# Performance work log

Measured on AMD Instinct MI355X. Metric: run time of the kernel, lower is better.

Reference implementation:

```python
import jax, jax.numpy as jnp
import numpy as np

EMB, HID, VOC, NLAYERS, TLEN = 256, 512, 32000, 2, 64
SRC_LEN, BS = 128, 64
DEC_HID = 2 * HID  # decoder hidden = hidden_dim * 2


def _p(key, shape, scale=0.05):
    return jax.random.normal(key, shape, dtype=jnp.float32) * scale


def setup_inputs() -> dict:
    key = jax.random.key(0)
    ks = jax.random.split(key, 24)
    d = {}
    d["sentences"] = jax.random.randint(ks[0], (SRC_LEN, BS), 0, VOC)
    d["targets"] = jax.random.randint(ks[1], (TLEN, BS), 0, VOC)
    d["emb"] = _p(ks[2], (VOC, EMB))
    # encoder: bidirectional, 2 layers; gate order i,f,g,o (PyTorch)
    d["enc0_Wih"] = _p(ks[3], (2, 4 * HID, EMB))
    d["enc0_Whh"] = _p(ks[4], (2, 4 * HID, HID))
    d["enc0_bih"] = _p(ks[5], (2, 4 * HID))
    d["enc0_bhh"] = _p(ks[6], (2, 4 * HID))
    d["enc1_Wih"] = _p(ks[7], (2, 4 * HID, 2 * HID))
    d["enc1_Whh"] = _p(ks[8], (2, 4 * HID, HID))
    d["enc1_bih"] = _p(ks[9], (2, 4 * HID))
    d["enc1_bhh"] = _p(ks[10], (2, 4 * HID))
    # decoder: unidirectional, 2 layers, hidden DEC_HID
    d["dec0_Wih"] = _p(ks[11], (4 * DEC_HID, EMB))
    d["dec0_Whh"] = _p(ks[12], (4 * DEC_HID, DEC_HID))
    d["dec0_bih"] = _p(ks[13], (4 * DEC_HID,))
    d["dec0_bhh"] = _p(ks[14], (4 * DEC_HID,))
    d["dec1_Wih"] = _p(ks[15], (4 * DEC_HID, DEC_HID))
    d["dec1_Whh"] = _p(ks[16], (4 * DEC_HID, DEC_HID))
    d["dec1_bih"] = _p(ks[17], (4 * DEC_HID,))
    d["dec1_bhh"] = _p(ks[18], (4 * DEC_HID,))
    d["W_out"] = _p(ks[19], (VOC, DEC_HID))
    d["b_out"] = _p(ks[20], (VOC,))
    return d


def lstm_scan(x, h0, c0, Wih, Whh, bih, bhh, reverse=False):
    # x: (T,B,In). Precompute input projection for the whole sequence.
    xw = jnp.einsum('tbi,gi->tbg', x, Wih) + bih  # (T,B,4H)

    def step(carry, g_in):
        h, c = carry
        g = g_in + h @ Whh.T + bhh
        i, f, gg, o = jnp.split(g, 4, axis=-1)
        c = jax.nn.sigmoid(f) * c + jax.nn.sigmoid(i) * jnp.tanh(gg)
        h = jax.nn.sigmoid(o) * jnp.tanh(c)
        return (h, c), h

    (hT, cT), ys = jax.lax.scan(step, (h0, c0), xw, reverse=reverse)
    return ys, hT, cT


def _forward(sentences, targets, emb,
             enc0_Wih, enc0_Whh, enc0_bih, enc0_bhh,
             enc1_Wih, enc1_Whh, enc1_bih, enc1_bhh,
             dec0_Wih, dec0_Whh, dec0_bih, dec0_bhh,
             dec1_Wih, dec1_Whh, dec1_bih, dec1_bhh,
             W_out, b_out):
    bs = sentences.shape[1]
    x = emb[sentences]  # (S,B,E)
    z = jnp.zeros((bs, HID), jnp.float32)
    enc_layers = ((enc0_Wih, enc0_Whh, enc0_bih, enc0_bhh),
                  (enc1_Wih, enc1_Whh, enc1_bih, enc1_bhh))
    hs, cs = [], []
    for Wih, Whh, bih, bhh in enc_layers:
        yf, hf, cf = lstm_scan(x, z, z, Wih[0], Whh[0], bih[0], bhh[0])
        yb, hb, cb = lstm_scan(x, z, z, Wih[1], Whh[1], bih[1], bhh[1], reverse=True)
        x = jnp.concatenate([yf, yb], axis=-1)  # (S,B,2H)
        hs.append(jnp.concatenate([hf, hb], axis=-1))  # _reshape_hidden concat
        cs.append(jnp.concatenate([cf, cb], axis=-1))
    # teacher forcing: decoder inputs are last source token, then targets[:-1]
    dec_tokens = jnp.concatenate([sentences[-1:], targets[:-1]], axis=0)  # (T,B)
    y = emb[dec_tokens]  # (T,B,E); dropout is identity in eval mode
    dec_layers = ((dec0_Wih, dec0_Whh, dec0_bih, dec0_bhh),
                  (dec1_Wih, dec1_Whh, dec1_bih, dec1_bhh))
    for l, (Wih, Whh, bih, bhh) in enumerate(dec_layers):
        y, _, _ = lstm_scan(y, hs[l], cs[l], Wih, Whh, bih, bhh)
    logits = jnp.einsum('tbh,vh->tbv', y, W_out) + b_out  # (T,B,V)
    return jax.nn.log_softmax(logits, axis=-1)


def reference(sentences, targets, emb,
              enc0_Wih, enc0_Whh, enc0_bih, enc0_bhh,
              enc1_Wih, enc1_Whh, enc1_bih, enc1_bhh,
              dec0_Wih, dec0_Whh, dec0_bih, dec0_bhh,
              dec1_Wih, dec1_Whh, dec1_bih, dec1_bhh,
              W_out, b_out):
    return _forward(sentences, targets, emb,
                    enc0_Wih, enc0_Whh, enc0_bih, enc0_bhh,
                    enc1_Wih, enc1_Whh, enc1_bih, enc1_bhh,
                    dec0_Wih, dec0_Whh, dec0_bih, dec0_bhh,
                    dec1_Wih, dec1_Whh, dec1_bih, dec1_bhh,
                    W_out, b_out)
```

## Files before the change

kernel.cpp:

```cpp
#include <hip/hip_runtime.h>

#define S_LEN 128
#define T_LEN 64
#define BSZ   64
#define EMBD  256
#define HID_  512
#define DHID_ 1024
#define VOC_  32000
#define HSTR  1024

typedef float  f4_t  __attribute__((ext_vector_type(4)));
typedef float  f32x4 __attribute__((ext_vector_type(4)));
typedef short  s16x8 __attribute__((ext_vector_type(8)));
typedef __bf16 bf16x8 __attribute__((ext_vector_type(8)));
typedef unsigned short u16x4 __attribute__((ext_vector_type(4)));
typedef int    i32x2 __attribute__((ext_vector_type(2)));

#define WS_XWA  0ull
#define WS_XWB  (WS_XWA + 16777216ull)
#define WS_CS   (WS_XWB + 16777216ull)
#define WS_BAR  (WS_CS  + 131072ull)
#define WS_BF   (WS_BAR + 32768ull)
#define U_X0B   0ull
#define U_HE0   (U_X0B + 2097152ull)
#define U_HE1   (U_HE0 + 8388608ull)
#define U_HD0   (U_HE1 + 8388608ull)
#define U_HD1   (U_HD0 + 4194304ull)
#define U_HSB   (U_HD1 + 4194304ull)
#define U_E0W   (U_HSB + 131072ull)
#define U_E1W   (U_E0W + 1048576ull)
#define U_D0W   (U_E1W + 4194304ull)
#define U_D1W   (U_D0W + 1048576ull)

__device__ __forceinline__ unsigned short f2bf(float x) {
    unsigned u = __builtin_bit_cast(unsigned, x);
    return (unsigned short)((u + 0x7fffu + ((u >> 16) & 1u)) >> 16);
}

__device__ __forceinline__ f4_t sc_load4(const void* p) {
    f4_t v;
    asm volatile("global_load_dwordx4 %0, %1, off sc0 sc1" : "=v"(v) : "v"(p));
    return v;
}
__device__ __forceinline__ int sc_load1(const int* p) {
    int v;
    asm volatile("global_load_dword %0, %1, off sc0 sc1\n\ts_waitcnt vmcnt(0)"
                 : "=v"(v) : "v"(p) : "memory");
    return v;
}
__device__ __forceinline__ void sc_store_int(int* p, int v) {
    asm volatile("global_store_dword %0, %1, off sc0 sc1" :: "v"(p), "v"(v) : "memory");
}
__device__ __forceinline__ void sc_store8(void* p, i32x2 v) {
    asm volatile("global_store_dwordx2 %0, %1, off sc0 sc1" :: "v"(p), "v"(v) : "memory");
}
__device__ __forceinline__ float g_load1(const float* p) {
    float v;
    asm volatile("global_load_dword %0, %1, off" : "=v"(v) : "v"(p));
    return v;
}
__device__ __forceinline__ void wait_vm0() {
    asm volatile("s_waitcnt vmcnt(0)" ::: "memory");
}
__device__ __forceinline__ void wait_vm8() {
    asm volatile("s_waitcnt vmcnt(8)" ::: "memory");
}

__device__ __forceinline__ void gload_lds16(const void* g, void* l) {
    __builtin_amdgcn_global_load_lds(
        (const __attribute__((address_space(1))) void*)g,
        (__attribute__((address_space(3))) void*)l, 16, 0, 0);
}

__device__ __forceinline__ float sigmoidf_(float x) { return 1.f / (1.f + expf(-x)); }

__global__ __launch_bounds__(256) void f2b_kernel(
    const float* __restrict__ in, unsigned short* __restrict__ out, int n4)
{
    const int stride = gridDim.x * 256;
    for (int i = blockIdx.x * 256 + threadIdx.x; i < n4; i += stride) {
        const float4 v = reinterpret_cast<const float4*>(in)[i];
        u16x4 o = { f2bf(v.x), f2bf(v.y), f2bf(v.z), f2bf(v.w) };
        reinterpret_cast<u16x4*>(out)[i] = o;
    }
}

__global__ __launch_bounds__(64) void embed_src_kernel(
    const int* __restrict__ toks, const float* __restrict__ emb,
    unsigned short* __restrict__ out)
{
    const int i = blockIdx.x;
    const int tok = toks[i];
    const float4 v = reinterpret_cast<const float4*>(emb + (size_t)tok * EMBD)[threadIdx.x];
    u16x4 o = { f2bf(v.x), f2bf(v.y), f2bf(v.z), f2bf(v.w) };
    reinterpret_cast<u16x4*>(out + (size_t)i * EMBD)[threadIdx.x] = o;
}

__global__ __launch_bounds__(64) void embed_dec_kernel(
    const int* __restrict__ sent, const int* __restrict__ targ,
    const float* __restrict__ emb, unsigned short* __restrict__ out)
{
    const int i = blockIdx.x;
    const int t = i >> 6, b = i & 63;
    const int tok = (t == 0) ? sent[(S_LEN - 1) * BSZ + b] : targ[(t - 1) * BSZ + b];
    const float4 v = reinterpret_cast<const float4*>(emb + (size_t)tok * EMBD)[threadIdx.x];
    u16x4 o = { f2bf(v.x), f2bf(v.y), f2bf(v.z), f2bf(v.w) };
    reinterpret_cast<u16x4*>(out + (size_t)i * EMBD)[threadIdx.x] = o;
}

__global__ __launch_bounds__(256) void gemm_bf16_kernel(
    const unsigned short* __restrict__ A, const unsigned short* __restrict__ B,
    const float* __restrict__ b1, const float* __restrict__ b2,
    float* __restrict__ C, int M, int N, int K, int nTN, int tmode,
    float* __restrict__ part)
{
    __shared__ __align__(16) unsigned short As[128 * 64];
    __shared__ __align__(16) unsigned short Bs[128 * 64];
    __shared__ float prt[2][128][2];

    const int tid  = threadIdx.x;
    const int lane = tid & 63;
    const int wv   = tid >> 6;
    const int wm   = wv >> 1, wn = wv & 1;

    const int nwg = gridDim.x;
    const int q = nwg >> 3, r = nwg & 7;
    const int xcd = blockIdx.x & 7, io = blockIdx.x >> 3;
    const int wg = (xcd < r ? xcd * (q + 1) : r * (q + 1) + (xcd - r) * q) + io;
    const int bm = (wg / nTN) * 128;
    const int bn = (wg % nTN) * 128;

    f32x4 acc[4][4];
#pragma unroll
    for (int i = 0; i < 4; ++i)
#pragma unroll
        for (int j = 0; j < 4; ++j) acc[i][j] = (f32x4)0.f;

    const int lin_base = wv * 1024 + lane * 16;

    for (int k0 = 0; k0 < K; k0 += 64) {
        __syncthreads();
#pragma unroll
        for (int qc = 0; qc < 4; ++qc) {
            const int lin = qc * 4096 + lin_base;
            const int row = lin >> 7;
            const int c   = (lin >> 4) & 7;
            const int sc  = c ^ (row & 7);
            const size_t gofs  = (size_t)(bm + row) * K + k0 + sc * 8;
            const size_t gofsB = (size_t)(bn + row) * K + k0 + sc * 8;
            char* ldst  = (char*)As + qc * 4096 + wv * 1024;
            char* ldstB = (char*)Bs + qc * 4096 + wv * 1024;
            gload_lds16(A + gofs, ldst);
            gload_lds16(B + gofsB, ldstB);
        }
        asm volatile("s_waitcnt vmcnt(0)" ::: "memory");
        __syncthreads();
#pragma unroll
        for (int ks = 0; ks < 2; ++ks) {
            bf16x8 af[4], bfv[4];
            const int ca = ks * 4 + (lane >> 4);
#pragma unroll
            for (int f = 0; f < 4; ++f) {
                const int ra = wm * 64 + f * 16 + (lane & 15);
                af[f] = __builtin_bit_cast(bf16x8,
                    *(const s16x8*)((const char*)As + ra * 128 + ((ca ^ (ra & 7)) << 4)));
                const int rb = wn * 64 + f * 16 + (lane & 15);
                bfv[f] = __builtin_bit_cast(bf16x8,
                    *(const s16x8*)((const char*)Bs + rb * 128 + ((ca ^ (rb & 7)) << 4)));
            }
#pragma unroll
            for (int i = 0; i < 4; ++i)
#pragma unroll
                for (int j = 0; j < 4; ++j)
                    acc[i][j] = __builtin_amdgcn_mfma_f32_16x16x32_bf16(
                        af[i], bfv[j], acc[i][j], 0, 0, 0);
        }
    }

    const int col0 = bn + wn * 64 + (lane & 15);
    if (tmode == 0) {
        const int row0 = bm + wm * 64 + ((lane >> 4) << 2);
        float bs[4];
#pragma unroll
        for (int j = 0; j < 4; ++j) {
            const int col = col0 + j * 16;
            bs[j] = b1[col];
            if (b2) bs[j] += b2[col];
        }
#pragma unroll
        for (int i = 0; i < 4; ++i)
#pragma unroll
            for (int j = 0; j < 4; ++j)
#pragma unroll
                for (int rg = 0; rg < 4; ++rg)
                    C[(size_t)(row0 + i * 16 + rg) * N + col0 + j * 16] = acc[i][j][rg] + bs[j];

        if (part) {
            float pm[4][4], ps[4][4];
#pragma unroll
            for (int i = 0; i < 4; ++i)
#pragma unroll
                for (int rg = 0; rg < 4; ++rg) {
                    float m = acc[i][0][rg] + bs[0];
                    m = fmaxf(m, acc[i][1][rg] + bs[1]);
                    m = fmaxf(m, acc[i][2][rg] + bs[2]);
                    m = fmaxf(m, acc[i][3][rg] + bs[3]);
                    pm[i][rg] = m;
                }
#pragma unroll
            for (int mask = 1; mask <= 8; mask <<= 1)
#pragma unroll
                for (int i = 0; i < 4; ++i)
#pragma unroll
                    for (int rg = 0; rg < 4; ++rg)
                        pm[i][rg] = fmaxf(pm[i][rg], __shfl_xor(pm[i][rg], mask));
#pragma unroll
            for (int i = 0; i < 4; ++i)
#pragma unroll
                for (int rg = 0; rg < 4; ++rg) {
                    float s = 0.f;
#pragma unroll
                    for (int j = 0; j < 4; ++j)
                        s += expf(acc[i][j][rg] + bs[j] - pm[i][rg]);
                    ps[i][rg] = s;
                }
#pragma unroll
            for (int mask = 1; mask <= 8; mask <<= 1)
#pragma unroll
                for (int i = 0; i < 4; ++i)
#pragma unroll
                    for (int rg = 0; rg < 4; ++rg)
                        ps[i][rg] += __shfl_xor(ps[i][rg], mask);
            if ((lane & 15) == 0) {
#pragma unroll
                for (int i = 0; i < 4; ++i)
#pragma unroll
                    for (int rg = 0; rg < 4; ++rg) {
                        const int r64 = ((lane >> 4) << 2) + i * 16 + rg;
                        prt[wn][wm * 64 + r64][0] = pm[i][rg];
                        prt[wn][wm * 64 + r64][1] = ps[i][rg];
                    }
            }
            __syncthreads();
            if (tid < 128) {
                const float m0_ = prt[0][tid][0], s0_ = prt[0][tid][1];
                const float m1_ = prt[1][tid][0], s1_ = prt[1][tid][1];
                const float Mx = fmaxf(m0_, m1_);
                const float Sx = s0_ * expf(m0_ - Mx) + s1_ * expf(m1_ - Mx);
                const size_t o = ((size_t)(bm + tid) * nTN + (bn >> 7)) * 2;
                part[o] = Mx; part[o + 1] = Sx;
            }
        }
    } else {
        const int tblk = (bm >> 6) + wm;
        const int rb = (lane >> 4) << 2;
#pragma unroll
        for (int i = 0; i < 4; ++i) {
#pragma unroll
            for (int j = 0; j < 4; ++j) {
                const int col = col0 + j * 16;
                float bias = b1[col];
                if (b2) bias += b2[col];
                float4 v = { acc[i][j][0] + bias, acc[i][j][1] + bias,
                             acc[i][j][2] + bias, acc[i][j][3] + bias };
                *reinterpret_cast<float4*>(&C[((size_t)tblk * N + col) * 64 + rb + i * 16]) = v;
            }
        }
    }
}

template<int H_T>
__global__ __launch_bounds__(256, 1) void lstm_mfma_scan(
    const float* __restrict__ xw0, const float* __restrict__ xw1,
    const float* __restrict__ Whh0, const float* __restrict__ Whh1,
    const unsigned short* __restrict__ h0b, const float* __restrict__ c0,
    unsigned short* __restrict__ hist,
    unsigned short* __restrict__ hsb, float* __restrict__ csd,
    int T, int ndir, int rev_mask, int* bar)
{
    constexpr int KST = H_T / 32;
    constexpr int CH  = H_T / 8;
    constexpr int NB  = (64 * CH) / 2048;

    __shared__ __align__(16) unsigned short h_lds[64 * H_T];
    __shared__ float pre[64][17];
    __shared__ __align__(8) unsigned short hpack[64][4];

    const int tid  = threadIdx.x;
    const int lane = tid & 63;
    const int w    = tid >> 6;
    const int bpd  = (ndir == 2) ? 128 : 256;
    const int dir  = blockIdx.x / bpd;
    const int blk  = blockIdx.x - dir * bpd;
    const int m0   = blk * 4;
    const int rev  = (rev_mask >> dir) & 1;
    const float* xw  = dir ? xw1  : xw0;
    const float* Whh = dir ? Whh1 : Whh0;
    const int dcol = dir * H_T;
    const int b = tid & 63;
    const int j = tid >> 6;

    int* myflag = bar + blockIdx.x * 32;
    const int* pollflag = bar + (dir * bpd + (tid < bpd ? tid : 0)) * 32;
    const bool polls = (tid < bpd);

    const int n  = lane & 15;
    const int kg = lane >> 4;
    const int wr = (n >> 2) * H_T + m0 + (n & 3);
    s16x8 wfr[KST];
#pragma unroll
    for (int ks = 0; ks < KST; ++ks) {
        const float* wp = Whh + (size_t)wr * H_T + ks * 32 + kg * 8;
        const float4 lo = *reinterpret_cast<const float4*>(wp);
        const float4 hi = *reinterpret_cast<const float4*>(wp + 4);
        s16x8 rr;
        rr[0] = (short)f2bf(lo.x); rr[1] = (short)f2bf(lo.y);
        rr[2] = (short)f2bf(lo.z); rr[3] = (short)f2bf(lo.w);
        rr[4] = (short)f2bf(hi.x); rr[5] = (short)f2bf(hi.y);
        rr[6] = (short)f2bf(hi.z); rr[7] = (short)f2bf(hi.w);
        wfr[ks] = rr;
    }

    float c  = c0 ? c0[(size_t)b * HSTR + dcol + m0 + j] : 0.f;
    float hn = 0.f;
    const int rA  = w * 16 + n;
    const int rAx = rA & 7;

    for (int s = 0; s < T; ++s) {
        const int tt = rev ? (T - 1 - s) : s;

        const float* xb = xw + ((size_t)tt * 4096 + m0 + j) * 64 + b;
        float xg0 = g_load1(xb);
        float xg1 = g_load1(xb + (size_t)H_T * 64);
        float xg2 = g_load1(xb + (size_t)2 * H_T * 64);
        float xg3 = g_load1(xb + (size_t)3 * H_T * 64);

        if (s > 0) {
            int ok = polls ? 0 : 1;
            for (;;) {
                if (!ok) ok = (sc_load1(pollflag) >= s) ? 1 : 0;
                if (__syncthreads_and(ok)) break;
            }
        }

        const unsigned short* hb;
        size_t tofs;
        if (s == 0) { hb = h0b; tofs = 0; }
        else {
            const int tp = rev ? (tt + 1) : (tt - 1);
            hb = hist; tofs = (size_t)tp * (64 * 1024);
        }

        float p0 = 0.f, p1 = 0.f, p2 = 0.f, p3 = 0.f;
        if (hb) {
            f4_t bufA[8], bufB[8];
            auto issue = [&](f4_t (&bf)[8], int bt) {
#pragma unroll
                for (int jj = 0; jj < 8; ++jj) {
                    const int idx = (bt * 8 + jj) * 256 + tid;
                    const int rr_ = idx / CH, cc_ = idx % CH;
                    bf[jj] = sc_load4(hb + tofs + (size_t)rr_ * 1024 + dcol + cc_ * 8);
                }
            };
            auto writeb = [&](const f4_t (&bf)[8], int bt) {
#pragma unroll
                for (int jj = 0; jj < 8; ++jj) {
                    const int idx = (bt * 8 + jj) * 256 + tid;
                    const int rr_ = idx / CH, cc_ = idx % CH;
                    const int off = rr_ * (2 * H_T) + ((cc_ ^ (rr_ & 7)) << 4);
                    *(f4_t*)((char*)h_lds + off) = bf[jj];
                }
            };
            issue(bufA, 0);
            if (NB > 1) issue(bufB, 1);
#pragma unroll
            for (int bt = 0; bt < NB; ++bt) {
                if (bt + 1 < NB) wait_vm8(); else wait_vm0();
                if (bt & 1) writeb(bufB, bt); else writeb(bufA, bt);
                if (bt + 2 < NB) { if (bt & 1) issue(bufB, bt + 2); else issue(bufA, bt + 2); }
            }
            __syncthreads();

            f32x4 acc = {0.f, 0.f, 0.f, 0.f};
#pragma unroll
            for (int ks = 0; ks < KST; ++ks) {
                const int cc_ = ks * 4 + kg;
                const int off = rA * (2 * H_T) + ((cc_ ^ rAx) << 4);
                const bf16x8 a = __builtin_bit_cast(bf16x8,
                    *(const s16x8*)((const char*)h_lds + off));
                acc = __builtin_amdgcn_mfma_f32_16x16x32_bf16(
                    a, __builtin_bit_cast(bf16x8, wfr[ks]), acc, 0, 0, 0);
            }
            __syncthreads();
#pragma unroll
            for (int rg = 0; rg < 4; ++rg)
                pre[w * 16 + kg * 4 + rg][n] = acc[rg];
            __syncthreads();
            p0 = pre[b][0 + j]; p1 = pre[b][4 + j];
            p2 = pre[b][8 + j]; p3 = pre[b][12 + j];
        }

        asm volatile("s_waitcnt vmcnt(0)"
                     : "+v"(xg0), "+v"(xg1), "+v"(xg2), "+v"(xg3) :: "memory");

        const float ig = sigmoidf_(p0 + xg0);
        const float fg = sigmoidf_(p1 + xg1);
        const float gg = tanhf(p2 + xg2);
        const float og = sigmoidf_(p3 + xg3);
        c  = fg * c + ig * gg;
        hn = og * tanhf(c);

        hpack[b][j] = f2bf(hn);
        __syncthreads();
        if (tid < 64) {
            const i32x2 v2 = *reinterpret_cast<const i32x2*>(&hpack[tid][0]);
            sc_store8(hist + (size_t)tt * (64 * 1024) + (size_t)tid * 1024 + dcol + m0, v2);
        }
        wait_vm0();
        __syncthreads();
        if (s + 1 < T && tid == 0) sc_store_int(myflag, s + 1);
    }

    if (hsb) hsb[(size_t)b * 1024 + dcol + m0 + j] = f2bf(hn);
    if (csd) csd[(size_t)b * HSTR + dcol + m0 + j] = c;
}

__global__ __launch_bounds__(256) void lsm_merge_kernel(
    const float* __restrict__ part, float* __restrict__ ml, int nt)
{
    __shared__ float ms[256], ss[256];
    const int tid = threadIdx.x;
    float m = -3.0e38f, s = 0.f;
    for (int t = tid; t < nt; t += 256) {
        const float mo = part[((size_t)blockIdx.x * nt + t) * 2];
        const float so = part[((size_t)blockIdx.x * nt + t) * 2 + 1];
        const float M = fmaxf(m, mo);
        s = s * expf(m - M) + so * expf(mo - M);
        m = M;
    }
    ms[tid] = m; ss[tid] = s;
    __syncthreads();
    for (int off = 128; off > 0; off >>= 1) {
        if (tid < off) {
            const float m2 = ms[tid + off], s2 = ss[tid + off];
            const float m1 = ms[tid],       s1 = ss[tid];
            const float M = fmaxf(m1, m2);
            ss[tid] = s1 * expf(m1 - M) + s2 * expf(m2 - M);
            ms[tid] = M;
        }
        __syncthreads();
    }
    if (tid == 0) ml[blockIdx.x] = ms[0] + logf(ss[0]);
}

__global__ __launch_bounds__(256) void lsm_norm_kernel(
    float* __restrict__ x, const float* __restrict__ ml, int n4)
{
    const float ML = ml[blockIdx.x];
    float4* p = reinterpret_cast<float4*>(x + (size_t)blockIdx.x * (n4 * 4));
    for (int cc = threadIdx.x; cc < n4; cc += 256) {
        float4 v = p[cc];
        v.x -= ML; v.y -= ML; v.z -= ML; v.w -= ML;
        p[cc] = v;
    }
}

extern "C" void kernel_launch(void* const* d_in, const int* in_sizes, int n_in,
                              void* d_out, int out_size, void* d_ws, size_t ws_size,
                              hipStream_t stream)
{
    const int*   sent  = (const int*)d_in[0];
    const int*   targ  = (const int*)d_in[1];
    const float* emb   = (const float*)d_in[2];
    const float* e0Wih = (const float*)d_in[3];
    const float* e0Whh = (const float*)d_in[4];
    const float* e0bih = (const float*)d_in[5];
    const float* e0bhh = (const float*)d_in[6];
    const float* e1Wih = (const float*)d_in[7];
    const float* e1Whh = (const float*)d_in[8];
    const float* e1bih = (const float*)d_in[9];
    const float* e1bhh = (const float*)d_in[10];
    const float* d0Wih = (const float*)d_in[11];
    const float* d0Whh = (const float*)d_in[12];
    const float* d0bih = (const float*)d_in[13];
    const float* d0bhh = (const float*)d_in[14];
    const float* d1Wih = (const float*)d_in[15];
    const float* d1Whh = (const float*)d_in[16];
    const float* d1bih = (const float*)d_in[17];
    const float* d1bhh = (const float*)d_in[18];
    const float* Wout  = (const float*)d_in[19];
    const float* bout  = (const float*)d_in[20];

    float* ws  = (float*)d_ws;
    float* xwA = ws + WS_XWA;
    float* xwB = ws + WS_XWB;
    float* cs  = ws + WS_CS;
    int*   bar = (int*)(ws + WS_BAR);
    unsigned short* ub    = (unsigned short*)(ws + WS_BF);
    unsigned short* x0b   = ub + U_X0B;
    unsigned short* h_e0  = ub + U_HE0;
    unsigned short* h_e1  = ub + U_HE1;
    unsigned short* h_d0  = ub + U_HD0;
    unsigned short* h_d1  = ub + U_HD1;
    unsigned short* hsb   = ub + U_HSB;
    unsigned short* e0Wb  = ub + U_E0W;
    unsigned short* e1Wb  = ub + U_E1W;
    unsigned short* d0Wb  = ub + U_D0W;
    unsigned short* d1Wb  = ub + U_D1W;
    unsigned short* Woutb = (unsigned short*)xwA;
    float* out = (float*)d_out;
    float* ml  = cs;

    hipMemsetAsync(bar, 0, 4 * 8192 * sizeof(int), stream);

    f2b_kernel<<<256, 256, 0, stream>>>(e0Wih, e0Wb, 1048576 / 4);
    f2b_kernel<<<512, 256, 0, stream>>>(e1Wih, e1Wb, 4194304 / 4);
    f2b_kernel<<<256, 256, 0, stream>>>(d0Wih, d0Wb, 1048576 / 4);
    f2b_kernel<<<512, 256, 0, stream>>>(d1Wih, d1Wb, 4194304 / 4);

    embed_src_kernel<<<S_LEN * BSZ, 64, 0, stream>>>(sent, emb, x0b);
    gemm_bf16_kernel<<<64 * 32, 256, 0, stream>>>(x0b, e0Wb, e0bih, e0bhh, xwA,
                                                  S_LEN * BSZ, 4096, EMBD, 32, 1, nullptr);
    lstm_mfma_scan<512><<<256, 256, 0, stream>>>(xwA, xwA + 2048 * 64,
                                                 e0Whh, e0Whh + 2048ull * 512,
                                                 nullptr, nullptr, h_e0,
                                                 hsb, cs, S_LEN, 2, 2, bar);
    gemm_bf16_kernel<<<64 * 32, 256, 0, stream>>>(h_e0, e1Wb, e1bih, e1bhh, xwA,
                                                  S_LEN * BSZ, 4096, 2 * HID_, 32, 1, nullptr);
    lstm_mfma_scan<512><<<256, 256, 0, stream>>>(xwA, xwA + 2048 * 64,
                                                 e1Whh, e1Whh + 2048ull * 512,
                                                 nullptr, nullptr, h_e1,
                                                 hsb + 65536, cs + 65536,
                                                 S_LEN, 2, 2, bar + 8192);
    embed_dec_kernel<<<T_LEN * BSZ, 64, 0, stream>>>(sent, targ, emb, x0b);
    gemm_bf16_kernel<<<32 * 32, 256, 0, stream>>>(x0b, d0Wb, d0bih, d0bhh, xwA,
                                                  T_LEN * BSZ, 4 * DHID_, EMBD, 32, 1, nullptr);
    lstm_mfma_scan<1024><<<256, 256, 0, stream>>>(xwA, nullptr, d0Whh, nullptr,
                                                  hsb, cs, h_d0,
                                                  nullptr, nullptr, T_LEN, 1, 0,
                                                  bar + 2 * 8192);
    f2b_kernel<<<2048, 256, 0, stream>>>(Wout, Woutb, (VOC_ * DHID_) / 4);
    gemm_bf16_kernel<<<32 * 32, 256, 0, stream>>>(h_d0, d1Wb, d1bih, d1bhh, xwB,
                                                  T_LEN * BSZ, 4 * DHID_, DHID_, 32, 1, nullptr);
    lstm_mfma_scan<1024><<<256, 256, 0, stream>>>(xwB, nullptr, d1Whh, nullptr,
                                                  hsb + 65536, cs + 65536, h_d1,
                                                  nullptr, nullptr, T_LEN, 1, 0,
                                                  bar + 3 * 8192);
    gemm_bf16_kernel<<<32 * 250, 256, 0, stream>>>(h_d1, Woutb, bout, nullptr, out,
                                                   T_LEN * BSZ, VOC_, DHID_, 250, 0, xwB);
    lsm_merge_kernel<<<T_LEN * BSZ, 256, 0, stream>>>(xwB, ml, 250);
    lsm_norm_kernel<<<T_LEN * BSZ, 256, 0, stream>>>(out, ml, VOC_ / 4);
}
```

Measured before the change: 2.679 ms.

## Merge conversion launches, fuse log-softmax stages, drop scan barriers, widen embed blocks

Four bf16 weight conversions now run in one launch, and the log-softmax merge and normalize kernels are fused into one. The embedding kernels use 256-thread blocks that each cover four tokens. Two __syncthreads are removed from the LSTM scan step, one before the pre-activation write to shared memory and one after the history store. Dropping those barriers saves per-step sync cost but risks LDS races between iterations, since the pre and hpack buffers are reused without a barrier.

```diff
diff --git a/kernel.cpp b/kernel.cpp
--- a/kernel.cpp
+++ b/kernel.cpp
@@ -74,6 +74,25 @@
 
 __device__ __forceinline__ float sigmoidf_(float x) { return 1.f / (1.f + expf(-x)); }
 
+__global__ __launch_bounds__(256) void f2b_multi_kernel(
+    const float* __restrict__ p0, unsigned short* __restrict__ q0,
+    const float* __restrict__ p1, unsigned short* __restrict__ q1,
+    const float* __restrict__ p2, unsigned short* __restrict__ q2,
+    const float* __restrict__ p3, unsigned short* __restrict__ q3)
+{
+    const int stride = gridDim.x * 256;
+    for (int i = blockIdx.x * 256 + threadIdx.x; i < 2621440; i += stride) {
+        const float* in; unsigned short* out; int o;
+        if (i < 262144)       { in = p0; out = q0; o = i; }
+        else if (i < 1310720) { in = p1; out = q1; o = i - 262144; }
+        else if (i < 1572864) { in = p2; out = q2; o = i - 1310720; }
+        else                  { in = p3; out = q3; o = i - 1572864; }
+        const float4 v = reinterpret_cast<const float4*>(in)[o];
+        u16x4 w = { f2bf(v.x), f2bf(v.y), f2bf(v.z), f2bf(v.w) };
+        reinterpret_cast<u16x4*>(out)[o] = w;
+    }
+}
+
 __global__ __launch_bounds__(256) void f2b_kernel(
     const float* __restrict__ in, unsigned short* __restrict__ out, int n4)
 {
@@ -85,27 +104,29 @@
     }
 }
 
-__global__ __launch_bounds__(64) void embed_src_kernel(
+__global__ __launch_bounds__(256) void embed_src_kernel(
     const int* __restrict__ toks, const float* __restrict__ emb,
     unsigned short* __restrict__ out)
 {
-    const int i = blockIdx.x;
+    const int i = blockIdx.x * 4 + (threadIdx.x >> 6);
+    const int lane = threadIdx.x & 63;
     const int tok = toks[i];
-    const float4 v = reinterpret_cast<const float4*>(emb + (size_t)tok * EMBD)[threadIdx.x];
+    const float4 v = reinterpret_cast<const float4*>(emb + (size_t)tok * EMBD)[lane];
     u16x4 o = { f2bf(v.x), f2bf(v.y), f2bf(v.z), f2bf(v.w) };
-    reinterpret_cast<u16x4*>(out + (size_t)i * EMBD)[threadIdx.x] = o;
-}
-
-__global__ __launch_bounds__(64) void embed_dec_kernel(
+    reinterpret_cast<u16x4*>(out + (size_t)i * EMBD)[lane] = o;
+}
+
+__global__ __launch_bounds__(256) void embed_dec_kernel(
     const int* __restrict__ sent, const int* __restrict__ targ,
     const float* __restrict__ emb, unsigned short* __restrict__ out)
 {
-    const int i = blockIdx.x;
+    const int i = blockIdx.x * 4 + (threadIdx.x >> 6);
+    const int lane = threadIdx.x & 63;
     const int t = i >> 6, b = i & 63;
     const int tok = (t == 0) ? sent[(S_LEN - 1) * BSZ + b] : targ[(t - 1) * BSZ + b];
-    const float4 v = reinterpret_cast<const float4*>(emb + (size_t)tok * EMBD)[threadIdx.x];
+    const float4 v = reinterpret_cast<const float4*>(emb + (size_t)tok * EMBD)[lane];
     u16x4 o = { f2bf(v.x), f2bf(v.y), f2bf(v.z), f2bf(v.w) };
-    reinterpret_cast<u16x4*>(out + (size_t)i * EMBD)[threadIdx.x] = o;
+    reinterpret_cast<u16x4*>(out + (size_t)i * EMBD)[lane] = o;
 }
 
 __global__ __launch_bounds__(256) void gemm_bf16_kernel(
@@ -391,7 +412,6 @@
                 acc = __builtin_amdgcn_mfma_f32_16x16x32_bf16(
                     a, __builtin_bit_cast(bf16x8, wfr[ks]), acc, 0, 0, 0);
             }
-            __syncthreads();
 #pragma unroll
             for (int rg = 0; rg < 4; ++rg)
                 pre[w * 16 + kg * 4 + rg][n] = acc[rg];
@@ -417,7 +437,6 @@
             sc_store8(hist + (size_t)tt * (64 * 1024) + (size_t)tid * 1024 + dcol + m0, v2);
         }
         wait_vm0();
-        __syncthreads();
         if (s + 1 < T && tid == 0) sc_store_int(myflag, s + 1);
     }
 
@@ -425,8 +444,8 @@
     if (csd) csd[(size_t)b * HSTR + dcol + m0 + j] = c;
 }
 
-__global__ __launch_bounds__(256) void lsm_merge_kernel(
-    const float* __restrict__ part, float* __restrict__ ml, int nt)
+__global__ __launch_bounds__(256) void lsm_norm_kernel(
+    float* __restrict__ x, const float* __restrict__ part, int nt, int n4)
 {
     __shared__ float ms[256], ss[256];
     const int tid = threadIdx.x;
@@ -450,15 +469,9 @@
         }
         __syncthreads();
     }
-    if (tid == 0) ml[blockIdx.x] = ms[0] + logf(ss[0]);
-}
-
-__global__ __launch_bounds__(256) void lsm_norm_kernel(
-    float* __restrict__ x, const float* __restrict__ ml, int n4)
-{
-    const float ML = ml[blockIdx.x];
+    const float ML = ms[0] + logf(ss[0]);
     float4* p = reinterpret_cast<float4*>(x + (size_t)blockIdx.x * (n4 * 4));
-    for (int cc = threadIdx.x; cc < n4; cc += 256) {
+    for (int cc = tid; cc < n4; cc += 256) {
         float4 v = p[cc];
         v.x -= ML; v.y -= ML; v.z -= ML; v.w -= ML;
         p[cc] = v;
@@ -509,16 +522,13 @@
     unsigned short* d1Wb  = ub + U_D1W;
     unsigned short* Woutb = (unsigned short*)xwA;
     float* out = (float*)d_out;
-    float* ml  = cs;
 
     hipMemsetAsync(bar, 0, 4 * 8192 * sizeof(int), stream);
 
-    f2b_kernel<<<256, 256, 0, stream>>>(e0Wih, e0Wb, 1048576 / 4);
-    f2b_kernel<<<512, 256, 0, stream>>>(e1Wih, e1Wb, 4194304 / 4);
-    f2b_kernel<<<256, 256, 0, stream>>>(d0Wih, d0Wb, 1048576 / 4);
-    f2b_kernel<<<512, 256, 0, stream>>>(d1Wih, d1Wb, 4194304 / 4);
-
-    embed_src_kernel<<<S_LEN * BSZ, 64, 0, stream>>>(sent, emb, x0b);
+    f2b_multi_kernel<<<1280, 256, 0, stream>>>(e0Wih, e0Wb, e1Wih, e1Wb,
+                                               d0Wih, d0Wb, d1Wih, d1Wb);
+
+    embed_src_kernel<<<(S_LEN * BSZ) / 4, 256, 0, stream>>>(sent, emb, x0b);
     gemm_bf16_kernel<<<64 * 32, 256, 0, stream>>>(x0b, e0Wb, e0bih, e0bhh, xwA,
                                                   S_LEN * BSZ, 4096, EMBD, 32, 1, nullptr);
     lstm_mfma_scan<512><<<256, 256, 0, stream>>>(xwA, xwA + 2048 * 64,
@@ -532,7 +542,7 @@
                                                  nullptr, nullptr, h_e1,
                                                  hsb + 65536, cs + 65536,
                                                  S_LEN, 2, 2, bar + 8192);
-    embed_dec_kernel<<<T_LEN * BSZ, 64, 0, stream>>>(sent, targ, emb, x0b);
+    embed_dec_kernel<<<(T_LEN * BSZ) / 4, 256, 0, stream>>>(sent, targ, emb, x0b);
     gemm_bf16_kernel<<<32 * 32, 256, 0, stream>>>(x0b, d0Wb, d0bih, d0bhh, xwA,
                                                   T_LEN * BSZ, 4 * DHID_, EMBD, 32, 1, nullptr);
     lstm_mfma_scan<1024><<<256, 256, 0, stream>>>(xwA, nullptr, d0Whh, nullptr,
@@ -548,6 +558,5 @@
                                                   bar + 3 * 8192);
     gemm_bf16_kernel<<<32 * 250, 256, 0, stream>>>(h_d1, Woutb, bout, nullptr, out,
                                                    T_LEN * BSZ, VOC_, DHID_, 250, 0, xwB);
-    lsm_merge_kernel<<<T_LEN * BSZ, 256, 0, stream>>>(xwB, ml, 250);
-    lsm_norm_kernel<<<T_LEN * BSZ, 256, 0, stream>>>(out, ml, VOC_ / 4);
-}
+    lsm_norm_kernel<<<T_LEN * BSZ, 256, 0, stream>>>(out, xwB, 250, VOC_ / 4);
+}
```

Result: no change. 2.637 ms (-1.6%).
